# Kernel tuning notes

Measured on AMD Instinct MI355X. Metric: run time of the kernel, lower is better.

## Reference

```python
import math
import jax, jax.numpy as jnp
import numpy as np

B, L, D, H = 2, 2048, 1024, 16
DH = D // H

def setup_inputs() -> dict:
    key = jax.random.key(0)
    ks = jax.random.split(key, 8)
    def xavier(k, fan_in, fan_out, shape):
        lim = math.sqrt(6.0 / (fan_in + fan_out))
        return jax.random.uniform(k, shape, jnp.float32, -lim, lim)
    x = jax.random.normal(ks[0], (B, L, D), jnp.float32)
    mask = jnp.ones((B, L), jnp.int32)
    # weights stored (in, out) so y = x @ W + b (equivalent to torch Linear)
    W_qkv = xavier(ks[1], D, 3 * D, (D, 3 * D))
    b_qkv = jnp.zeros((3 * D,), jnp.float32)
    W_out = xavier(ks[2], D, D, (D, D))
    b_out = jnp.zeros((D,), jnp.float32)
    W_phase = xavier(ks[3], D, H, (D, H))
    b_phase = jax.random.normal(ks[4], (H,), jnp.float32) * 0.02
    resonance_scale = jnp.float32(0.1)
    phase_scale = jnp.float32(1.0)
    return {"x": x, "mask": mask, "W_qkv": W_qkv, "b_qkv": b_qkv,
            "W_out": W_out, "b_out": b_out, "W_phase": W_phase,
            "b_phase": b_phase, "resonance_scale": resonance_scale,
            "phase_scale": phase_scale}

def reference(x, mask, W_qkv, b_qkv, W_out, b_out, W_phase, b_phase,
              resonance_scale, phase_scale):
    # qkv: (B,L,3D) -> (3,B,H,L,dh)
    qkv = (x @ W_qkv + b_qkv).reshape(B, L, 3, H, DH).transpose(2, 0, 3, 1, 4)
    q, k, v = qkv[0], qkv[1], qkv[2]
    scores = jnp.einsum('bhqd,bhkd->bhqk', q, k) / math.sqrt(DH)
    # per-token per-head phase (B,H,L)
    phase_val = jnp.tanh(phase_scale * (x @ W_phase + b_phase)).transpose(0, 2, 1)
    phase_diff = (phase_val[:, :, :, None] - phase_val[:, :, None, :]) ** 2
    scores = scores - resonance_scale * phase_diff
    # mask: (B,L) -> (B,1,1,L)
    m = mask[:, None, None, :]
    scores = jnp.where(m == 0, jnp.float32(-1e9), scores)
    attn = jax.nn.softmax(scores, axis=-1)
    out = jnp.einsum('bhqk,bhkd->bhqd', attn, v)  # (B,H,L,dh)
    out = out.transpose(0, 2, 1, 3).reshape(B, L, D)
    return out @ W_out + b_out
```

## Files before the change

kernel.cpp:

```cpp
#include <hip/hip_runtime.h>

typedef unsigned short u16;
typedef unsigned int u32;
typedef __attribute__((ext_vector_type(2))) unsigned long long u64x2;
typedef __attribute__((ext_vector_type(4))) unsigned short u16x4;
typedef __attribute__((ext_vector_type(8))) __bf16 bf16x8;
typedef __attribute__((ext_vector_type(4))) float f32x4;
typedef __attribute__((ext_vector_type(2))) float f32x2;

#define DEV static __device__ __forceinline__
#define LOG2E 1.4426950408889634f

DEV u16 f2bf(float f) { __bf16 h = (__bf16)f; return __builtin_bit_cast(u16, h); }

#define BB   2
#define LLEN 2048
#define DDIM 1024
#define HH   16
#define DH   64
#define MTOT 4096
#define N3   3072

DEV void gl16(const void* g, void* l) {
  __builtin_amdgcn_global_load_lds(
      (const __attribute__((address_space(1))) void*)g,
      (__attribute__((address_space(3))) void*)l, 16, 0, 0);
}

DEV void stage64(const u16* org, size_t gsb, u16* lds, int lane, int wid) {
#pragma unroll
  for (int j = 0; j < 2; j++) {
    int inst = wid * 2 + j;
    int r8 = lane >> 3;
    int row = inst * 8 + r8;
    int s = (r8 & 3) | ((inst & 1) << 2);
    const char* src = (const char*)org + (size_t)row * gsb +
                      (((lane & 7) ^ s) << 4);
    gl16(src, (char*)lds + inst * 1024);
  }
}
DEV bf16x8 read128s(const u16* tile, int row, int colb) {
  return *reinterpret_cast<const bf16x8*>(
      (const char*)tile + row * 128 +
      (colb ^ (((row & 3) | (((row >> 3) & 1) << 2)) << 4)));
}

DEV void stage128x32(const u16* org, size_t gsb, u16* lds, int lane, int wid) {
#pragma unroll
  for (int j = 0; j < 2; j++) {
    int inst = wid + j * 4;
    int r16 = lane >> 2;
    const char* src = (const char*)org + (size_t)(inst * 16 + r16) * gsb +
                      ((((lane & 3) ^ (r16 & 3))) << 4);
    gl16(src, (char*)lds + inst * 1024);
  }
}
DEV bf16x8 read64(const u16* tile, int row, int colb) {
  return *reinterpret_cast<const bf16x8*>(
      (const char*)tile + row * 64 + (colb ^ ((row & 3) << 4)));
}

__global__ __launch_bounds__(256) void k_cvt(const float* __restrict__ in,
                                             u16* __restrict__ out, int n) {
  int i = (blockIdx.x * 256 + threadIdx.x) * 4;
  if (i < n) {
    f32x4 v = *reinterpret_cast<const f32x4*>(in + i);
    u16x4 o;
    o.x = f2bf(v.x); o.y = f2bf(v.y); o.z = f2bf(v.z); o.w = f2bf(v.w);
    *reinterpret_cast<u16x4*>(out + i) = o;
  }
}

__global__ __launch_bounds__(256) void k_transpose_w(const float* __restrict__ W,
                                                     u16* __restrict__ WT,
                                                     int K, int N) {
  __shared__ float s[32][33];
  int k0 = blockIdx.x * 32, n0 = blockIdx.y * 32;
  int tx = threadIdx.x & 31, ty = threadIdx.x >> 5;
#pragma unroll
  for (int i = 0; i < 4; i++)
    s[ty + i * 8][tx] = W[(k0 + ty + i * 8) * (size_t)N + n0 + tx];
  __syncthreads();
#pragma unroll
  for (int i = 0; i < 4; i++)
    WT[(size_t)(n0 + ty + i * 8) * K + k0 + tx] = f2bf(s[tx][ty + i * 8]);
}

__global__ __launch_bounds__(256) void k_phase(const float* __restrict__ x,
                                               const float* __restrict__ Wp,
                                               const float* __restrict__ bp,
                                               const float* __restrict__ pscale,
                                               const float* __restrict__ rscale,
                                               const int* __restrict__ mask,
                                               f32x2* __restrict__ ppk) {
  int m = blockIdx.x;
  int t = threadIdx.x;
  int h = t & 15, j = t >> 4;
  const float* xr = x + (size_t)m * DDIM;
  float acc = 0.f;
#pragma unroll 4
  for (int kk = 0; kk < 64; kk++) {
    int k = j * 64 + kk;
    acc += xr[k] * Wp[k * HH + h];
  }
  __shared__ float s[16][17];
  s[j][h] = acc;
  __syncthreads();
  if (t < 16) {
    float sum = 0.f;
#pragma unroll
    for (int jj = 0; jj < 16; jj++) sum += s[jj][t];
    float v = tanhf((*pscale) * (sum + bp[t]));
    int b = m >> 11, l = m & (LLEN - 1);
    float kb = (mask[m] == 0) ? -1.0e9f : (-(*rscale) * LOG2E) * v * v;
    f32x2 o; o.x = v; o.y = kb;
    ppk[((size_t)(b * HH + t)) * LLEN + l] = o;
  }
}

template <bool BF16_OUT>
__global__ __launch_bounds__(256) void k_gemm(const u16* __restrict__ A,
                                              const u16* __restrict__ BT,
                                              const float* __restrict__ bias,
                                              void* __restrict__ C,
                                              int M, int N, int K) {
  __shared__ __attribute__((aligned(16))) u16 sA[2][128 * 32];
  __shared__ __attribute__((aligned(16))) u16 sB[2][128 * 32];
  int m0 = blockIdx.x * 128, n0 = blockIdx.y * 128;
  int t = threadIdx.x, lane = t & 63, wid = t >> 6;
  int wm = wid >> 1, wn = wid & 1;
  int lc = lane & 15, lg = lane >> 4;

  const u16* Ao = A + (size_t)m0 * K;
  const u16* Bo = BT + (size_t)n0 * K;

  f32x4 acc[4][4] = {};
  stage128x32(Ao, (size_t)K * 2, sA[0], lane, wid);
  stage128x32(Bo, (size_t)K * 2, sB[0], lane, wid);
  __syncthreads();
  int cur = 0;
  int NT = K >> 5;
  for (int kt = 0; kt < NT; kt++) {
    if (kt + 1 < NT) {
      stage128x32(Ao + (kt + 1) * 32, (size_t)K * 2, sA[cur ^ 1], lane, wid);
      stage128x32(Bo + (kt + 1) * 32, (size_t)K * 2, sB[cur ^ 1], lane, wid);
    }
    bf16x8 af[4], bfr[4];
#pragma unroll
    for (int i = 0; i < 4; i++) af[i] = read64(sA[cur], wm * 64 + i * 16 + lc, lg * 16);
#pragma unroll
    for (int j = 0; j < 4; j++) bfr[j] = read64(sB[cur], wn * 64 + j * 16 + lc, lg * 16);
    __builtin_amdgcn_s_setprio(1);
#pragma unroll
    for (int i = 0; i < 4; i++)
#pragma unroll
      for (int j = 0; j < 4; j++)
        acc[i][j] = __builtin_amdgcn_mfma_f32_16x16x32_bf16(af[i], bfr[j], acc[i][j], 0, 0, 0);
    __builtin_amdgcn_s_setprio(0);
    __syncthreads();
    cur ^= 1;
  }

  int rg = lane >> 4;
#pragma unroll
  for (int i = 0; i < 4; i++) {
#pragma unroll
    for (int j = 0; j < 4; j++) {
      int col = n0 + wn * 64 + j * 16 + lc;
      float bv = bias[col];
#pragma unroll
      for (int r = 0; r < 4; r++) {
        int row = m0 + wm * 64 + i * 16 + rg * 4 + r;
        float v = acc[i][j][r] + bv;
        if (BF16_OUT)
          ((u16*)C)[(size_t)row * N + col] = f2bf(v);
        else
          ((float*)C)[(size_t)row * N + col] = v;
      }
    }
  }
}

__global__ __launch_bounds__(256) void k_vtrans(const u16* __restrict__ qkv,
                                                u16* __restrict__ vT) {
  int bh = blockIdx.y;
  int lt = blockIdx.x;
  int b = bh >> 4, h = bh & 15;
  __shared__ __attribute__((aligned(16))) u16 s[64][72];
  int t = threadIdx.x;
#pragma unroll
  for (int i = 0; i < 2; i++) {
    int c = t + i * 256;
    int l = c >> 3, ko = (c & 7) * 8;
    *reinterpret_cast<u64x2*>(&s[l][ko]) = *reinterpret_cast<const u64x2*>(
        &qkv[(size_t)(b * LLEN + lt * 64 + l) * N3 + 2 * DDIM + h * DH + ko]);
  }
  __syncthreads();
#pragma unroll
  for (int i = 0; i < 2; i++) {
    int c = t + i * 256;
    int dh = c >> 3, lo = (c & 7) * 8;
    u16 tmp[8];
#pragma unroll
    for (int j = 0; j < 8; j++) tmp[j] = s[lo + j][dh];
    *reinterpret_cast<u64x2*>(&vT[((size_t)bh * DH + dh) * LLEN + lt * 64 + lo]) =
        *reinterpret_cast<u64x2*>(tmp);
  }
}

__global__ __launch_bounds__(256, 4) void k_attn(const u16* __restrict__ qkv,
                                                 const u16* __restrict__ vT,
                                                 const f32x2* __restrict__ ppk,
                                                 const float* __restrict__ rscale_p,
                                                 u16* __restrict__ attn_out) {
  __shared__ __attribute__((aligned(16))) u16 kS[2][64 * 64];
  __shared__ __attribute__((aligned(16))) u16 vS[2][64 * 64];

  int bh = blockIdx.y, b = bh >> 4, h = bh & 15;
  int q0 = blockIdx.x * 64;
  int t = threadIdx.x, lane = t & 63, wid = t >> 6;
  int qb = q0 + wid * 16;
  int lc = lane & 15, lg = lane >> 4;

  const float rs2 = (*rscale_p) * LOG2E;
  const float c1 = 0.125f * LOG2E;
  const f32x2* pprow = ppk + (size_t)bh * LLEN;

  bf16x8 qf0, qf1;
  {
    const u16* qp = &qkv[(size_t)(b * LLEN + qb + lc) * N3 + h * DH + lg * 8];
    qf0 = *reinterpret_cast<const bf16x8*>(qp);
    qf1 = *reinterpret_cast<const bf16x8*>(qp + 32);
  }
  float wq = 2.f * rs2 * pprow[qb + lc].x;

  const u16* kg = qkv + (size_t)(b * LLEN) * N3 + DDIM + h * DH;
  const u16* vg = vT + (size_t)bh * DH * LLEN;

  stage64(kg, (size_t)N3 * 2, kS[0], lane, wid);
  stage64(vg, (size_t)LLEN * 2, vS[0], lane, wid);

  f32x4 o[4] = {};
  float mrow = -1e30f, lrow = 0.f;
  int arow = ((lc >> 2) << 3) | (lc & 3);

  __syncthreads();
  int cur = 0;
  for (int kt = 0; kt < LLEN / 64; kt++) {
    int kb = kt * 64;
    if (kt + 1 < LLEN / 64) {
      stage64(kg + (size_t)(kb + 64) * N3, (size_t)N3 * 2, kS[cur ^ 1], lane, wid);
      stage64(vg + kb + 64, (size_t)LLEN * 2, vS[cur ^ 1], lane, wid);
    }

    f32x4 ph[4][2];
#pragma unroll
    for (int blk = 0; blk < 4; blk++) {
      int off = kb + ((blk & 2) << 4) + ((blk & 1) << 2) + lg * 8;
      ph[blk][0] = *reinterpret_cast<const f32x4*>(&pprow[off]);
      ph[blk][1] = *reinterpret_cast<const f32x4*>(&pprow[off + 2]);
    }

    f32x4 sv[4];
#pragma unroll
    for (int blk = 0; blk < 4; blk++) {
      int krow = arow + ((blk & 2) << 4) + ((blk & 1) << 2);
      bf16x8 kf0 = read128s(kS[cur], krow, lg * 16);
      bf16x8 kf1 = read128s(kS[cur], krow, 64 + lg * 16);
      f32x4 z = {};
      __builtin_amdgcn_s_setprio(1);
      z = __builtin_amdgcn_mfma_f32_16x16x32_bf16(kf0, qf0, z, 0, 0, 0);
      z = __builtin_amdgcn_mfma_f32_16x16x32_bf16(kf1, qf1, z, 0, 0, 0);
      __builtin_amdgcn_s_setprio(0);
      sv[blk] = z;
    }

#pragma unroll
    for (int blk = 0; blk < 4; blk++) {
#pragma unroll
      for (int r = 0; r < 4; r++) {
        f32x4 pp = ph[blk][r >> 1];
        float pk = (r & 1) ? pp.z : pp.x;
        float kbv = (r & 1) ? pp.w : pp.y;
        sv[blk][r] = fmaf(sv[blk][r], c1, fmaf(wq, pk, kbv));
      }
    }

    float rm = sv[0][0];
#pragma unroll
    for (int blk = 0; blk < 4; blk++)
#pragma unroll
      for (int r = 0; r < 4; r++) rm = fmaxf(rm, sv[blk][r]);
    rm = fmaxf(rm, __shfl_xor(rm, 16, 64));
    rm = fmaxf(rm, __shfl_xor(rm, 32, 64));

    if (!__all(rm <= mrow + 8.f)) {
      float mn = fmaxf(mrow, rm);
      float al = __builtin_amdgcn_exp2f(mrow - mn);
      mrow = mn;
      lrow *= al;
      float ao0 = __shfl(al, lg * 4 + 0, 16);
      float ao1 = __shfl(al, lg * 4 + 1, 16);
      float ao2 = __shfl(al, lg * 4 + 2, 16);
      float ao3 = __shfl(al, lg * 4 + 3, 16);
#pragma unroll
      for (int d = 0; d < 4; d++) {
        o[d][0] *= ao0; o[d][1] *= ao1; o[d][2] *= ao2; o[d][3] *= ao3;
      }
    }

    float ssum = 0.f;
#pragma unroll
    for (int blk = 0; blk < 4; blk++)
#pragma unroll
      for (int r = 0; r < 4; r++) {
        float p = __builtin_amdgcn_exp2f(sv[blk][r] - mrow);
        sv[blk][r] = p;
        ssum += p;
      }
    ssum += __shfl_xor(ssum, 16, 64);
    ssum += __shfl_xor(ssum, 32, 64);
    lrow += ssum;

    bf16x8 pa0, pa1;
#pragma unroll
    for (int r = 0; r < 4; r++) {
      pa0[r] = (__bf16)sv[0][r];
      pa0[4 + r] = (__bf16)sv[1][r];
      pa1[r] = (__bf16)sv[2][r];
      pa1[4 + r] = (__bf16)sv[3][r];
    }

#pragma unroll
    for (int d = 0; d < 4; d++) {
      bf16x8 vb0 = read128s(vS[cur], d * 16 + lc, lg * 16);
      bf16x8 vb1 = read128s(vS[cur], d * 16 + lc, 64 + lg * 16);
      __builtin_amdgcn_s_setprio(1);
      o[d] = __builtin_amdgcn_mfma_f32_16x16x32_bf16(pa0, vb0, o[d], 0, 0, 0);
      o[d] = __builtin_amdgcn_mfma_f32_16x16x32_bf16(pa1, vb1, o[d], 0, 0, 0);
      __builtin_amdgcn_s_setprio(0);
    }

    __syncthreads();
    cur ^= 1;
  }

  float linv = 1.0f / lrow;
  float li0 = __shfl(linv, lg * 4 + 0, 16);
  float li1 = __shfl(linv, lg * 4 + 1, 16);
  float li2 = __shfl(linv, lg * 4 + 2, 16);
  float li3 = __shfl(linv, lg * 4 + 3, 16);
#pragma unroll
  for (int d = 0; d < 4; d++) {
    int col = h * DH + d * 16 + lc;
    size_t base = (size_t)(b * LLEN + qb + lg * 4) * DDIM + col;
    attn_out[base] = f2bf(o[d][0] * li0);
    attn_out[base + DDIM] = f2bf(o[d][1] * li1);
    attn_out[base + 2 * DDIM] = f2bf(o[d][2] * li2);
    attn_out[base + 3 * DDIM] = f2bf(o[d][3] * li3);
  }
}

extern "C" void kernel_launch(void* const* d_in, const int* in_sizes, int n_in,
                              void* d_out, int out_size, void* d_ws, size_t ws_size,
                              hipStream_t stream) {
  const float* x       = (const float*)d_in[0];
  const int*   mask    = (const int*)d_in[1];
  const float* W_qkv   = (const float*)d_in[2];
  const float* b_qkv   = (const float*)d_in[3];
  const float* W_out   = (const float*)d_in[4];
  const float* b_out   = (const float*)d_in[5];
  const float* W_phase = (const float*)d_in[6];
  const float* b_phase = (const float*)d_in[7];
  const float* rscale  = (const float*)d_in[8];
  const float* pscale  = (const float*)d_in[9];
  float* out = (float*)d_out;

  char* ws = (char*)d_ws;
  u16* x_bf     = (u16*)(ws + 0);
  u16* wt_qkv   = (u16*)(ws + 8388608);
  u16* wt_out   = (u16*)(ws + 14680064);
  u16* qkv      = (u16*)(ws + 16777216);
  u16* vT       = (u16*)(ws + 41943040);
  u16* attn_out = (u16*)(ws + 50331648);
  f32x2* ppk    = (f32x2*)(ws + 58720256);

  k_cvt<<<MTOT * DDIM / 4 / 256, 256, 0, stream>>>(x, x_bf, MTOT * DDIM);
  k_transpose_w<<<dim3(DDIM / 32, N3 / 32), 256, 0, stream>>>(W_qkv, wt_qkv, DDIM, N3);
  k_transpose_w<<<dim3(DDIM / 32, DDIM / 32), 256, 0, stream>>>(W_out, wt_out, DDIM, DDIM);
  k_phase<<<MTOT, 256, 0, stream>>>(x, W_phase, b_phase, pscale, rscale, mask, ppk);
  k_gemm<true><<<dim3(MTOT / 128, N3 / 128), 256, 0, stream>>>(
      x_bf, wt_qkv, b_qkv, qkv, MTOT, N3, DDIM);
  k_vtrans<<<dim3(LLEN / 64, BB * HH), 256, 0, stream>>>(qkv, vT);
  k_attn<<<dim3(LLEN / 64, BB * HH), 256, 0, stream>>>(
      qkv, vT, ppk, rscale, attn_out);
  k_gemm<false><<<dim3(MTOT / 128, DDIM / 128), 256, 0, stream>>>(
      attn_out, wt_out, b_out, out, MTOT, DDIM, DDIM);
}
```

Baseline: 250.3 us.

## Stage phase terms through LDS and use explicit vmcnt waits with raw barriers

The per-key phase values (pk, kbias) move from direct global loads inside the attention loop to the double-buffered async global-to-LDS pipeline used for K and V. The __syncthreads calls become an explicit s_waitcnt vmcnt on the current tile plus a raw s_barrier, so the next tile's loads stay in flight across the barrier. This is meant to hide global-load latency for the phase vector and avoid draining all outstanding loads every iteration. The hand-counted vmcnt(6) has to match the exact number of issued loads, and the raw barriers drop the compiler's LDS fences, which adds correctness risk.

```diff
diff --git a/kernel.cpp b/kernel.cpp
--- a/kernel.cpp
+++ b/kernel.cpp
@@ -25,6 +25,11 @@
   __builtin_amdgcn_global_load_lds(
       (const __attribute__((address_space(1))) void*)g,
       (__attribute__((address_space(3))) void*)l, 16, 0, 0);
+}
+DEV void gl4(const void* g, void* l) {
+  __builtin_amdgcn_global_load_lds(
+      (const __attribute__((address_space(1))) void*)g,
+      (__attribute__((address_space(3))) void*)l, 4, 0, 0);
 }
 
 DEV void stage64(const u16* org, size_t gsb, u16* lds, int lane, int wid) {
@@ -215,6 +220,7 @@
                                                  u16* __restrict__ attn_out) {
   __shared__ __attribute__((aligned(16))) u16 kS[2][64 * 64];
   __shared__ __attribute__((aligned(16))) u16 vS[2][64 * 64];
+  __shared__ __attribute__((aligned(16))) float ppS[2][128];
 
   int bh = blockIdx.y, b = bh >> 4, h = bh & 15;
   int q0 = blockIdx.x * 64;
@@ -225,6 +231,7 @@
   const float rs2 = (*rscale_p) * LOG2E;
   const float c1 = 0.125f * LOG2E;
   const f32x2* pprow = ppk + (size_t)bh * LLEN;
+  const float* pprowf = (const float*)pprow;
 
   bf16x8 qf0, qf1;
   {
@@ -239,27 +246,28 @@
 
   stage64(kg, (size_t)N3 * 2, kS[0], lane, wid);
   stage64(vg, (size_t)LLEN * 2, vS[0], lane, wid);
+  gl4(pprowf + lane, &ppS[0][0]);
+  gl4(pprowf + 64 + lane, &ppS[0][64]);
 
   f32x4 o[4] = {};
   float mrow = -1e30f, lrow = 0.f;
   int arow = ((lc >> 2) << 3) | (lc & 3);
 
-  __syncthreads();
   int cur = 0;
-  for (int kt = 0; kt < LLEN / 64; kt++) {
+  const int NT = LLEN / 64;
+  for (int kt = 0; kt < NT; kt++) {
     int kb = kt * 64;
-    if (kt + 1 < LLEN / 64) {
+    if (kt + 1 < NT) {
       stage64(kg + (size_t)(kb + 64) * N3, (size_t)N3 * 2, kS[cur ^ 1], lane, wid);
       stage64(vg + kb + 64, (size_t)LLEN * 2, vS[cur ^ 1], lane, wid);
-    }
-
-    f32x4 ph[4][2];
-#pragma unroll
-    for (int blk = 0; blk < 4; blk++) {
-      int off = kb + ((blk & 2) << 4) + ((blk & 1) << 2) + lg * 8;
-      ph[blk][0] = *reinterpret_cast<const f32x4*>(&pprow[off]);
-      ph[blk][1] = *reinterpret_cast<const f32x4*>(&pprow[off + 2]);
-    }
+      const float* pt = pprowf + (size_t)(kb + 64) * 2;
+      gl4(pt + lane, &ppS[cur ^ 1][0]);
+      gl4(pt + 64 + lane, &ppS[cur ^ 1][64]);
+      asm volatile("s_waitcnt vmcnt(6)" ::: "memory");
+    } else {
+      asm volatile("s_waitcnt vmcnt(0)" ::: "memory");
+    }
+    __builtin_amdgcn_s_barrier();
 
     f32x4 sv[4];
 #pragma unroll
@@ -275,14 +283,17 @@
       sv[blk] = z;
     }
 
-#pragma unroll
-    for (int blk = 0; blk < 4; blk++) {
-#pragma unroll
-      for (int r = 0; r < 4; r++) {
-        f32x4 pp = ph[blk][r >> 1];
-        float pk = (r & 1) ? pp.z : pp.x;
-        float kbv = (r & 1) ? pp.w : pp.y;
-        sv[blk][r] = fmaf(sv[blk][r], c1, fmaf(wq, pk, kbv));
+    {
+      const float* pt = &ppS[cur][0];
+#pragma unroll
+      for (int blk = 0; blk < 4; blk++) {
+        int off2 = (((blk & 2) << 4) + ((blk & 1) << 2) + lg * 8) * 2;
+        f32x4 p0 = *reinterpret_cast<const f32x4*>(pt + off2);
+        f32x4 p1 = *reinterpret_cast<const f32x4*>(pt + off2 + 4);
+        sv[blk][0] = fmaf(sv[blk][0], c1, fmaf(wq, p0.x, p0.y));
+        sv[blk][1] = fmaf(sv[blk][1], c1, fmaf(wq, p0.z, p0.w));
+        sv[blk][2] = fmaf(sv[blk][2], c1, fmaf(wq, p1.x, p1.y));
+        sv[blk][3] = fmaf(sv[blk][3], c1, fmaf(wq, p1.z, p1.w));
       }
     }
 
@@ -341,7 +352,7 @@
       __builtin_amdgcn_s_setprio(0);
     }
 
-    __syncthreads();
+    __builtin_amdgcn_s_barrier();
     cur ^= 1;
   }
 
```

Result: faster. 234.9 us (-6.2%).
